# Optimization experiments

Measured on AMD Instinct MI355X. Metric: run time of the kernel, lower is better.

## Reference

```python
import jax, jax.numpy as jnp
import numpy as np

NUM_ITERATIONS = 3

def squash(t, axis=-1):
    sq = jnp.sum(t * t, axis=axis, keepdims=True)
    scale = sq / (1.0 + sq)
    return scale * t / jnp.sqrt(sq)

def setup_inputs() -> dict:
    key = jax.random.key(0)
    k1, k2 = jax.random.split(key)
    B, N, Ci = 16, 1024, 64
    C, O = 32, 32
    x = jax.random.normal(k1, (B, N, Ci), dtype=jnp.float32)
    route_weights = jax.random.normal(k2, (C, N, Ci, O), dtype=jnp.float32)
    return {"x": x, "route_weights": route_weights}

def reference(x, route_weights):
    # priors: (C, B, N, O)  == torch's (C,B,N,1,O) with singleton squeezed
    priors = jnp.einsum('bni,cnio->cbno', x, route_weights)
    C, B, N, O = priors.shape
    logits = jnp.zeros((C, B, N, 1), dtype=priors.dtype)
    outputs = None
    for i in range(NUM_ITERATIONS):
        probs = jax.nn.softmax(logits, axis=2)  # over route nodes
        outputs = squash(jnp.sum(probs * priors, axis=2, keepdims=True))  # (C,B,1,O)
        if i != NUM_ITERATIONS - 1:
            delta = jnp.sum(priors * outputs, axis=-1, keepdims=True)  # (C,B,N,1)
            logits = logits + delta
    # match torch output shape (C, B, 1, 1, O)
    return outputs[:, :, :, None, :]
```

## Files before the change

kernel.cpp:

```cpp
#include <hip/hip_runtime.h>

constexpr int kB  = 16;
constexpr int kN  = 1024;
constexpr int kCI = 64;
constexpr int kC  = 32;
constexpr int kO  = 32;
constexpr int kNT = 4;

__global__ __launch_bounds__(128) void priors_kernel(
    const float* __restrict__ x,
    const float* rw,
    float* priors, int nstride) {
  const int c  = blockIdx.x >> 8;
  const int n0 = (blockIdx.x & 255) * kNT;
  const int t  = threadIdx.x;

  __shared__ float ws[kNT * kCI * kO];
  __shared__ float xs[kNT * kCI * kB];

  {
    const float4* src = (const float4*)(rw + (size_t)(c * kN + n0) * (kCI * kO));
    float4* dst4 = (float4*)ws;
    #pragma unroll
    for (int it = 0; it < 16; ++it) {
      int f = t + 128 * it;
      dst4[f] = src[f];
    }
  }
  {
    #pragma unroll
    for (int it = 0; it < 8; ++it) {
      int f = t + 128 * it;
      int b = f & 15;
      int a = (f >> 4) & 15;
      int j = f >> 8;
      float4 v = *(const float4*)(x + (size_t)(b * kN + n0 + j) * kCI + a * 4);
      int idx = (j * kCI + a * 4) * kB + b;
      xs[idx +  0] = v.x;
      xs[idx + 16] = v.y;
      xs[idx + 32] = v.z;
      xs[idx + 48] = v.w;
    }
  }
  __syncthreads();

  const int j  = t >> 5;
  const int og = (t & 31) >> 2;
  const int bg = t & 3;
  const float* wp = ws + j * (kCI * kO) + og * 4;
  const float* xp = xs + j * (kCI * kB) + bg * 4;

  float acc[4][4];
  #pragma unroll
  for (int bb = 0; bb < 4; ++bb)
    #pragma unroll
    for (int oo = 0; oo < 4; ++oo) acc[bb][oo] = 0.f;

  #pragma unroll
  for (int i0 = 0; i0 < kCI; i0 += 4) {
    float4 wv[4], xv[4];
    #pragma unroll
    for (int q = 0; q < 4; ++q) wv[q] = *(const float4*)(wp + (i0 + q) * kO);
    #pragma unroll
    for (int q = 0; q < 4; ++q) xv[q] = *(const float4*)(xp + (i0 + q) * kB);
    #pragma unroll
    for (int q = 0; q < 4; ++q) {
      const float* xq = (const float*)&xv[q];
      const float* wq = (const float*)&wv[q];
      #pragma unroll
      for (int bb = 0; bb < 4; ++bb)
        #pragma unroll
        for (int oo = 0; oo < 4; ++oo)
          acc[bb][oo] += xq[bb] * wq[oo];
    }
  }

  float* dst = priors + (size_t)(c * kN + n0) * nstride;
  #pragma unroll
  for (int bb = 0; bb < 4; ++bb) {
    int b = bg * 4 + bb;
    float4 v = make_float4(acc[bb][0], acc[bb][1], acc[bb][2], acc[bb][3]);
    *(float4*)(dst + (size_t)j * nstride + b * kO + og * 4) = v;
  }
}

__global__ __launch_bounds__(256) void routing_kernel(
    const float* priors, int nstride,
    float* __restrict__ out) {
  const int cb = blockIdx.x;
  const int c = cb >> 4, b = cb & 15;
  const int t = threadIdx.x;

  __shared__ float R[256 * 33];
  __shared__ float S2[8 * 33];
  __shared__ float out_lds[kO];
  __shared__ float wred[8];

  const float* base = priors + (size_t)c * kN * nstride + b * kO;

  float p[4][kO];
  #pragma unroll
  for (int k = 0; k < 4; ++k) {
    const float* rp = base + (size_t)(t + 256 * k) * nstride;
    #pragma unroll
    for (int q = 0; q < 8; ++q) {
      float4 v = *(const float4*)(rp + q * 4);
      p[k][q * 4 + 0] = v.x; p[k][q * 4 + 1] = v.y;
      p[k][q * 4 + 2] = v.z; p[k][q * 4 + 3] = v.w;
    }
  }

  float l[4] = {0.f, 0.f, 0.f, 0.f};

  for (int iter = 0; iter < 3; ++iter) {
    if (iter > 0) {
      #pragma unroll
      for (int k = 0; k < 4; ++k) {
        float d = 0.f;
        #pragma unroll
        for (int o = 0; o < kO; ++o) d += p[k][o] * out_lds[o];
        l[k] += d;
      }
    }
    float lm = fmaxf(fmaxf(l[0], l[1]), fmaxf(l[2], l[3]));
    #pragma unroll
    for (int s = 32; s >= 1; s >>= 1) lm = fmaxf(lm, __shfl_xor(lm, s));
    if ((t & 63) == 0) wred[t >> 6] = lm;
    __syncthreads();
    const float m = fmaxf(fmaxf(wred[0], wred[1]), fmaxf(wred[2], wred[3]));

    float acc[kO];
    #pragma unroll
    for (int o = 0; o < kO; ++o) acc[o] = 0.f;
    float denp = 0.f;
    #pragma unroll
    for (int k = 0; k < 4; ++k) {
      float e = __expf(l[k] - m);
      denp += e;
      #pragma unroll
      for (int o = 0; o < kO; ++o) acc[o] += e * p[k][o];
    }
    #pragma unroll
    for (int s = 32; s >= 1; s >>= 1) denp += __shfl_xor(denp, s);
    if ((t & 63) == 0) wred[4 + (t >> 6)] = denp;

    #pragma unroll
    for (int o = 0; o < kO; ++o) R[t * 33 + o] = acc[o];
    __syncthreads();
    {
      int o = t & 31, g = t >> 5;
      float s = 0.f;
      #pragma unroll
      for (int jj = 0; jj < 32; ++jj) s += R[(g * 32 + jj) * 33 + o];
      S2[g * 33 + o] = s;
    }
    __syncthreads();
    if (t < kO) {
      float s = 0.f;
      #pragma unroll
      for (int g = 0; g < 8; ++g) s += S2[g * 33 + t];
      const float den = wred[4] + wred[5] + wred[6] + wred[7];
      s /= den;
      float sq = s * s;
      #pragma unroll
      for (int sh = 16; sh >= 1; sh >>= 1) sq += __shfl_xor(sq, sh);
      const float r = sqrtf(sq);
      const float ov = s * (r / (1.f + sq));
      out_lds[t] = ov;
      if (iter == 2) out[cb * kO + t] = ov;
    }
    __syncthreads();
  }
}

extern "C" void kernel_launch(void* const* d_in, const int* in_sizes, int n_in,
                              void* d_out, int out_size, void* d_ws, size_t ws_size,
                              hipStream_t stream) {
  const float* x  = (const float*)d_in[0];
  const float* rw = (const float*)d_in[1];
  float* out = (float*)d_out;

  const size_t need = (size_t)kC * kN * kB * kO * sizeof(float);
  float* priors;
  int nstride;
  if (ws_size >= need) {
    priors  = (float*)d_ws;
    nstride = kB * kO;
  } else {
    priors  = (float*)const_cast<float*>(rw);
    nstride = kCI * kO;
  }

  priors_kernel<<<dim3(kC * (kN / kNT)), dim3(128), 0, stream>>>(x, rw, priors, nstride);
  routing_kernel<<<dim3(kC * kB), dim3(256), 0, stream>>>(priors, nstride, out);
}
```

Measured before the change: 395.5 us.

## Load route weights via global_load_lds, read x directly, relayout priors per (c,b)

Weight tiles are now copied straight from global memory into LDS with the global_load_lds builtin instead of passing through registers. The x staging and transpose in LDS is removed, and x is read from global memory as float4 per batch row. In the workspace path the priors layout changes to (c,b,n,o), so each routing block reads a contiguous region. The direct x loads depend on cache reuse across threads, and the priors stores from the first kernel become more scattered.

```diff
diff --git a/kernel.cpp b/kernel.cpp
--- a/kernel.cpp
+++ b/kernel.cpp
@@ -7,16 +7,18 @@
 constexpr int kO  = 32;
 constexpr int kNT = 4;
 
+#define AS1(p) ((__attribute__((address_space(1))) void*)(p))
+#define AS3(p) ((__attribute__((address_space(3))) void*)(p))
+
 __global__ __launch_bounds__(128) void priors_kernel(
     const float* __restrict__ x,
     const float* rw,
-    float* priors, int nstride) {
+    float* priors, int cstride, int bstride, int nstr) {
   const int c  = blockIdx.x >> 8;
   const int n0 = (blockIdx.x & 255) * kNT;
   const int t  = threadIdx.x;
 
   __shared__ float ws[kNT * kCI * kO];
-  __shared__ float xs[kNT * kCI * kB];
 
   {
     const float4* src = (const float4*)(rw + (size_t)(c * kN + n0) * (kCI * kO));
@@ -24,22 +26,8 @@
     #pragma unroll
     for (int it = 0; it < 16; ++it) {
       int f = t + 128 * it;
-      dst4[f] = src[f];
-    }
-  }
-  {
-    #pragma unroll
-    for (int it = 0; it < 8; ++it) {
-      int f = t + 128 * it;
-      int b = f & 15;
-      int a = (f >> 4) & 15;
-      int j = f >> 8;
-      float4 v = *(const float4*)(x + (size_t)(b * kN + n0 + j) * kCI + a * 4);
-      int idx = (j * kCI + a * 4) * kB + b;
-      xs[idx +  0] = v.x;
-      xs[idx + 16] = v.y;
-      xs[idx + 32] = v.z;
-      xs[idx + 48] = v.w;
+      __builtin_amdgcn_global_load_lds(AS1(const_cast<float4*>(src + f)),
+                                       AS3(dst4 + f), 16, 0, 0);
     }
   }
   __syncthreads();
@@ -47,8 +35,8 @@
   const int j  = t >> 5;
   const int og = (t & 31) >> 2;
   const int bg = t & 3;
-  const float* wp = ws + j * (kCI * kO) + og * 4;
-  const float* xp = xs + j * (kCI * kB) + bg * 4;
+  const float* wp  = ws + j * (kCI * kO) + og * 4;
+  const float* xr0 = x + (size_t)(bg * 4) * (kN * kCI) + (size_t)(n0 + j) * kCI;
 
   float acc[4][4];
   #pragma unroll
@@ -62,30 +50,32 @@
     #pragma unroll
     for (int q = 0; q < 4; ++q) wv[q] = *(const float4*)(wp + (i0 + q) * kO);
     #pragma unroll
-    for (int q = 0; q < 4; ++q) xv[q] = *(const float4*)(xp + (i0 + q) * kB);
+    for (int bb = 0; bb < 4; ++bb)
+      xv[bb] = *(const float4*)(xr0 + (size_t)bb * (kN * kCI) + i0);
     #pragma unroll
     for (int q = 0; q < 4; ++q) {
-      const float* xq = (const float*)&xv[q];
       const float* wq = (const float*)&wv[q];
       #pragma unroll
-      for (int bb = 0; bb < 4; ++bb)
+      for (int bb = 0; bb < 4; ++bb) {
+        const float xq = ((const float*)&xv[bb])[q];
         #pragma unroll
         for (int oo = 0; oo < 4; ++oo)
-          acc[bb][oo] += xq[bb] * wq[oo];
+          acc[bb][oo] += xq * wq[oo];
+      }
     }
   }
 
-  float* dst = priors + (size_t)(c * kN + n0) * nstride;
+  float* dst = priors + (size_t)c * cstride + (size_t)(n0 + j) * nstr + og * 4;
   #pragma unroll
   for (int bb = 0; bb < 4; ++bb) {
     int b = bg * 4 + bb;
     float4 v = make_float4(acc[bb][0], acc[bb][1], acc[bb][2], acc[bb][3]);
-    *(float4*)(dst + (size_t)j * nstride + b * kO + og * 4) = v;
+    *(float4*)(dst + (size_t)b * bstride) = v;
   }
 }
 
 __global__ __launch_bounds__(256) void routing_kernel(
-    const float* priors, int nstride,
+    const float* priors, int cstride, int bstride, int nstr,
     float* __restrict__ out) {
   const int cb = blockIdx.x;
   const int c = cb >> 4, b = cb & 15;
@@ -96,12 +86,12 @@
   __shared__ float out_lds[kO];
   __shared__ float wred[8];
 
-  const float* base = priors + (size_t)c * kN * nstride + b * kO;
+  const float* base = priors + (size_t)c * cstride + (size_t)b * bstride;
 
   float p[4][kO];
   #pragma unroll
   for (int k = 0; k < 4; ++k) {
-    const float* rp = base + (size_t)(t + 256 * k) * nstride;
+    const float* rp = base + (size_t)(t + 256 * k) * nstr;
     #pragma unroll
     for (int q = 0; q < 8; ++q) {
       float4 v = *(const float4*)(rp + q * 4);
@@ -182,15 +172,21 @@
 
   const size_t need = (size_t)kC * kN * kB * kO * sizeof(float);
   float* priors;
-  int nstride;
+  int cstride, bstride, nstr;
   if (ws_size >= need) {
     priors  = (float*)d_ws;
-    nstride = kB * kO;
+    cstride = kB * kN * kO;
+    bstride = kN * kO;
+    nstr    = kO;
   } else {
     priors  = (float*)const_cast<float*>(rw);
-    nstride = kCI * kO;
+    cstride = kN * kCI * kO;
+    bstride = kO;
+    nstr    = kCI * kO;
   }
 
-  priors_kernel<<<dim3(kC * (kN / kNT)), dim3(128), 0, stream>>>(x, rw, priors, nstride);
-  routing_kernel<<<dim3(kC * kB), dim3(256), 0, stream>>>(priors, nstride, out);
+  priors_kernel<<<dim3(kC * (kN / kNT)), dim3(128), 0, stream>>>(
+      x, rw, priors, cstride, bstride, nstr);
+  routing_kernel<<<dim3(kC * kB), dim3(256), 0, stream>>>(
+      priors, cstride, bstride, nstr, out);
 }
```

Result: slower. 434.7 us (+9.9%).
